# Kernel tuning notes

Hardware: AMD Instinct MI355X
Metric: run time of the kernel (lower is better)

Reference implementation:

```python
import jax, jax.numpy as jnp
from jax import lax
import numpy as np

SEQ, BATCH, IN, H = 512, 256, 180, 8


def _lstm_layer(x, w_ih, w_hh, b_ih, b_hh):
    # x: [S, B, I]; PyTorch gate order: i, f, g, o stacked along 4H
    S, B, _ = x.shape
    Hh = w_hh.shape[1]
    # input contribution for all timesteps at once (one big GEMM)
    xg = jnp.einsum('sbi,gi->sbg', x, w_ih) + b_ih + b_hh  # [S, B, 4H]

    def step(carry, xt):
        h, c = carry
        g = xt + h @ w_hh.T  # [B, 4H]
        i, f, gg, o = jnp.split(g, 4, axis=-1)
        i = jax.nn.sigmoid(i)
        f = jax.nn.sigmoid(f)
        gg = jnp.tanh(gg)
        o = jax.nn.sigmoid(o)
        c = f * c + i * gg
        h = o * jnp.tanh(c)
        return (h, c), h

    init = (jnp.zeros((B, Hh), x.dtype), jnp.zeros((B, Hh), x.dtype))
    _, ys = lax.scan(step, init, xg)
    return ys  # [S, B, H]


def setup_inputs() -> dict:
    key = jax.random.key(0)
    ks = jax.random.split(key, 11)
    s = 1.0 / np.sqrt(H)  # PyTorch LSTM init scale
    return {
        'x': jax.random.normal(ks[0], (SEQ, BATCH, IN), jnp.float32),
        'w_ih0': jax.random.uniform(ks[1], (4 * H, IN), jnp.float32, -s, s),
        'w_hh0': jax.random.uniform(ks[2], (4 * H, H), jnp.float32, -s, s),
        'b_ih0': jax.random.uniform(ks[3], (4 * H,), jnp.float32, -s, s),
        'b_hh0': jax.random.uniform(ks[4], (4 * H,), jnp.float32, -s, s),
        'w_ih1': jax.random.uniform(ks[5], (4 * H, H), jnp.float32, -s, s),
        'w_hh1': jax.random.uniform(ks[6], (4 * H, H), jnp.float32, -s, s),
        'b_ih1': jax.random.uniform(ks[7], (4 * H,), jnp.float32, -s, s),
        'b_hh1': jax.random.uniform(ks[8], (4 * H,), jnp.float32, -s, s),
        'w_reg': jax.random.uniform(ks[9], (2, H), jnp.float32, -s, s),
        'b_reg': jax.random.uniform(ks[10], (2,), jnp.float32, -s, s),
    }


def reference(x, w_ih0, w_hh0, b_ih0, b_hh0, w_ih1, w_hh1, b_ih1, b_hh1, w_reg, b_reg):
    h1 = _lstm_layer(x, w_ih0, w_hh0, b_ih0, b_hh0)   # [S, B, H]
    h2 = _lstm_layer(h1, w_ih1, w_hh1, b_ih1, b_hh1)  # [S, B, H]
    S, B, Hh = h2.shape
    flat = h2.reshape(S * B, Hh)
    return flat @ w_reg.T + b_reg  # [S*B, 2]
```

## Files before the change

### kernel.cpp

```cpp
#include <hip/hip_runtime.h>

#define S_  512
#define B_  256
#define NIN 180

typedef float v2 __attribute__((ext_vector_type(2)));

#define SSIG  -1.4426950408889634f
#define STANH -2.8853900817779268f

#define QP_X1 0xB1
#define QP_X2 0x4E
#define QP_X3 0x1B
#define ROR4  0x124
#define ROR8  0x128

template<int CTRL>
__device__ __forceinline__ float dppf(float x) {
    return __uint_as_float((unsigned)__builtin_amdgcn_update_dpp(
        0, (int)__float_as_uint(x), CTRL, 0xF, 0xF, true));
}

#define ROTS8(h, r) do { \
    r[0] = (h); \
    r[1] = dppf<QP_X1>(h); \
    r[2] = dppf<QP_X2>(h); \
    r[3] = dppf<QP_X3>(h); \
    r[4] = dppf<ROR4>(h); \
    r[5] = dppf<QP_X1>(r[4]); \
    r[6] = dppf<QP_X2>(r[4]); \
    r[7] = dppf<QP_X3>(r[4]); \
} while (0)

__global__ __launch_bounds__(512) void xg_gemm(
    const float* __restrict__ x, const float* __restrict__ w,
    const float* __restrict__ bi, const float* __restrict__ bh,
    float* __restrict__ xg2)
{
    __shared__ float xs[2][4][256];

    const int tid  = threadIdx.x;
    const int lane = tid & 63;
    const int qb   = __builtin_amdgcn_readfirstlane((tid >> 6) & 1);
    const int rs   = tid >> 7;
    const int row  = rs * 64 + lane;
    const int s    = blockIdx.x;
    const bool ldr = (tid < 256);

    const float* xrp = x + ((size_t)s * B_ + tid) * NIN;

    float acc[16];
    #pragma unroll
    for (int k = 0; k < 16; ++k) acc[k] = 0.f;

    float4 rr[4];
    float4 x0;
    if (ldr) {
        x0    = *(const float4*)(xrp + 0);
        rr[1] = *(const float4*)(xrp + 4);
        rr[2] = *(const float4*)(xrp + 8);
        rr[3] = *(const float4*)(xrp + 12);
        rr[0] = *(const float4*)(xrp + 16);
        xs[0][0][tid] = x0.x; xs[0][1][tid] = x0.y;
        xs[0][2][tid] = x0.z; xs[0][3][tid] = x0.w;
    }
    __syncthreads();

    auto COMP = [&](int ii, int buf) {
        float xe0 = xs[buf][0][row];
        float xe1 = xs[buf][1][row];
        float xe2 = xs[buf][2][row];
        float xe3 = xs[buf][3][row];
        #pragma unroll
        for (int jj = 0; jj < 8; ++jj) {
            float4 wA = *(const float4*)(w + (size_t)(qb * 8 + jj) * NIN + 4 * ii);
            float4 wB = *(const float4*)(w + (size_t)((2 + qb) * 8 + jj) * NIN + 4 * ii);
            acc[2*jj]   = __builtin_fmaf(wA.x, xe0, acc[2*jj]);
            acc[2*jj+1] = __builtin_fmaf(wB.x, xe0, acc[2*jj+1]);
            acc[2*jj]   = __builtin_fmaf(wA.y, xe1, acc[2*jj]);
            acc[2*jj+1] = __builtin_fmaf(wB.y, xe1, acc[2*jj+1]);
            acc[2*jj]   = __builtin_fmaf(wA.z, xe2, acc[2*jj]);
            acc[2*jj+1] = __builtin_fmaf(wB.z, xe2, acc[2*jj+1]);
            acc[2*jj]   = __builtin_fmaf(wA.w, xe3, acc[2*jj]);
            acc[2*jj+1] = __builtin_fmaf(wB.w, xe3, acc[2*jj+1]);
        }
    };

    for (int base = 0; base <= 40; base += 4) {
        #pragma unroll
        for (int p = 0; p < 4; ++p) {
            const int ii = base + p;
            if (ldr && ii < 44) {
                const int sl = (p + 1) & 3;
                float4 wv = rr[sl];
                xs[(ii + 1) & 1][0][tid] = wv.x;
                xs[(ii + 1) & 1][1][tid] = wv.y;
                xs[(ii + 1) & 1][2][tid] = wv.z;
                xs[(ii + 1) & 1][3][tid] = wv.w;
                if (ii <= 39)
                    rr[sl] = *(const float4*)(xrp + 4 * (ii + 5));
            }
            COMP(ii, p & 1);
            __syncthreads();
        }
    }
    COMP(44, 0);

    float ob[16];
    #pragma unroll
    for (int c = 0; c < 2; ++c) {
        #pragma unroll
        for (int jj = 0; jj < 8; ++jj) {
            int g = (qb + 2 * c) * 8 + jj;
            float sc = (qb == 0 && c == 1) ? STANH : SSIG;
            ob[2*jj+c] = sc * acc[2*jj+c] + sc * (bi[g] + bh[g]);
        }
    }
    float* dst = xg2 + (((size_t)s * 64 + (row >> 2)) * 64
                        + (row & 3) * 16 + qb * 8) * 2;
    #pragma unroll
    for (int k = 0; k < 4; ++k) {
        float4 o = {ob[4*k], ob[4*k+1], ob[4*k+2], ob[4*k+3]};
        *(float4*)(dst + 4 * k) = o;
    }
}

__global__ __launch_bounds__(256, 1) void lstm_scan(
    const float* __restrict__ xg,
    const float* __restrict__ w_hh0,
    const float* __restrict__ w_ih1, const float* __restrict__ w_hh1,
    const float* __restrict__ b_ih1, const float* __restrict__ b_hh1,
    const float* __restrict__ w_reg, const float* __restrict__ b_reg,
    float* __restrict__ out)
{
    __shared__ float ring0[16][64];
    __shared__ float ring1[16][128];
    __shared__ float ring2[16][64];

    const int tid = threadIdx.x;
    const int wid = tid >> 6;
    const int lt  = tid & 63;
    const int j   = lt & 7;
    const int b3  = (lt >> 3) & 1;
    const int cc  = lt >> 4;
    const bool b3z = (b3 == 0);
    const int bid = blockIdx.x;

    const int gA = b3 * 8 + j;
    const int gB = (2 + b3) * 8 + j;
    const float sB_ = b3z ? STANH : SSIG;
    const float aB  = b3z ? 2.0f : 1.0f;
    const float bB  = b3z ? -1.0f : 0.0f;

    auto COMBINE2 = [&](float tA, float tB, float& c, float& h) {
        float m  = tA * tB;
        float mr = dppf<ROR8>(m);
        float fa = dppf<ROR8>(tA);
        float ob = dppf<ROR8>(tB);
        float ig = b3z ? m  : mr;
        float f  = b3z ? fa : tA;
        float o  = b3z ? ob : tB;
        c = __builtin_fmaf(f, c, ig);
        float th = __builtin_fmaf(2.0f, __builtin_amdgcn_rcpf(
            1.0f + __builtin_amdgcn_exp2f(STANH * c)), -1.0f);
        h = o * th;
    };

    if (wid == 0) {
        v2 w0p[8];
        #pragma unroll
        for (int m = 0; m < 8; ++m) {
            int k = j ^ m;
            w0p[m] = v2{SSIG * w_hh0[gA * 8 + k], sB_ * w_hh0[gB * 8 + k]};
        }
        float h0p = 0.f, c0v = 0.f;

        const float* xbase = xg + (size_t)bid * 128 + lt * 2;
        v2 xq[8];
        #pragma unroll
        for (int k = 0; k < 8; ++k) xq[k] = *(const v2*)(xbase + (size_t)k * 8192);

        for (int hh = 0; hh < 64; ++hh) {
            const float* pre = xbase + (size_t)((8 * hh + 8) & 511) * 8192;
            const int sb8 = (hh & 1) * 8;
            #pragma unroll
            for (int k = 0; k < 8; ++k) {
                v2 xc = xq[k];
                xq[k] = *(const v2*)(pre + (size_t)k * 8192);
                float r0[8];
                ROTS8(h0p, r0);
                v2 a0L = __builtin_elementwise_fma(w0p[0], v2{r0[0], r0[0]}, xc);
                v2 a0H = w0p[4] * v2{r0[4], r0[4]};
                #pragma unroll
                for (int m = 1; m < 4; ++m) {
                    a0L = __builtin_elementwise_fma(w0p[m], v2{r0[m], r0[m]}, a0L);
                    a0H = __builtin_elementwise_fma(w0p[m + 4], v2{r0[m + 4], r0[m + 4]}, a0H);
                }
                v2 a0 = a0L + a0H;
                float eA = __builtin_amdgcn_exp2f(a0.x);
                float eB = __builtin_amdgcn_exp2f(a0.y);
                float tA = __builtin_amdgcn_rcpf(1.0f + eA);
                float tB = __builtin_fmaf(aB, __builtin_amdgcn_rcpf(1.0f + eB), bB);
                COMBINE2(tA, tB, c0v, h0p);
                ring0[sb8 + k][lt] = h0p;
                if (k == 3 || k == 7) __syncthreads();
            }
        }
        __syncthreads();
        __syncthreads();
    } else if (wid == 1) {
        v2 wi1p[8];
        #pragma unroll
        for (int m = 0; m < 8; ++m) {
            int k = j ^ m;
            wi1p[m] = v2{SSIG * w_ih1[gA * 8 + k], sB_ * w_ih1[gB * 8 + k]};
        }
        const v2 b1p = v2{SSIG * (b_ih1[gA] + b_hh1[gA]),
                          sB_  * (b_ih1[gB] + b_hh1[gB])};

        __syncthreads();
        for (int p = 1; p <= 128; ++p) {
            const int sb = ((p - 1) & 3) * 4;
            float h0v[4];
            #pragma unroll
            for (int k = 0; k < 4; ++k) h0v[k] = ring0[sb + k][lt];
            #pragma unroll
            for (int k = 0; k < 4; ++k) {
                float r0[8];
                ROTS8(h0v[k], r0);
                v2 a = __builtin_elementwise_fma(wi1p[0], v2{r0[0], r0[0]}, b1p);
                #pragma unroll
                for (int m = 1; m < 8; ++m)
                    a = __builtin_elementwise_fma(wi1p[m], v2{r0[m], r0[m]}, a);
                *(v2*)&ring1[sb + k][lt * 2] = a;
            }
            __syncthreads();
        }
        __syncthreads();
    } else if (wid == 2) {
        v2 wh1p[8];
        #pragma unroll
        for (int m = 0; m < 8; ++m) {
            int k = j ^ m;
            wh1p[m] = v2{SSIG * w_hh1[gA * 8 + k], sB_ * w_hh1[gB * 8 + k]};
        }
        float h1p = 0.f, c1v = 0.f;

        auto BODY4 = [&](int p) {
            const int sb = ((p - 2) & 3) * 4;
            v2 a1in[4];
            #pragma unroll
            for (int k = 0; k < 4; ++k) a1in[k] = *(const v2*)&ring1[sb + k][lt * 2];
            #pragma unroll
            for (int k = 0; k < 4; ++k) {
                float r1[8];
                ROTS8(h1p, r1);
                v2 aL = __builtin_elementwise_fma(wh1p[0], v2{r1[0], r1[0]}, a1in[k]);
                v2 aH = wh1p[4] * v2{r1[4], r1[4]};
                #pragma unroll
                for (int m = 1; m < 4; ++m) {
                    aL = __builtin_elementwise_fma(wh1p[m], v2{r1[m], r1[m]}, aL);
                    aH = __builtin_elementwise_fma(wh1p[m + 4], v2{r1[m + 4], r1[m + 4]}, aH);
                }
                v2 a1 = aL + aH;
                float eA = __builtin_amdgcn_exp2f(a1.x);
                float eB = __builtin_amdgcn_exp2f(a1.y);
                float tA = __builtin_amdgcn_rcpf(1.0f + eA);
                float tB = __builtin_fmaf(aB, __builtin_amdgcn_rcpf(1.0f + eB), bB);
                COMBINE2(tA, tB, c1v, h1p);
                ring2[sb + k][lt] = h1p;
            }
        };

        __syncthreads();
        __syncthreads();
        for (int p = 2; p <= 128; ++p) { BODY4(p); __syncthreads(); }
        BODY4(129);
        __syncthreads();
    } else {
        float wrl[8];
        #pragma unroll
        for (int m = 0; m < 8; ++m) wrl[m] = w_reg[b3 * 8 + (j ^ m)];
        const float br  = b_reg[b3];
        const bool isl  = (j == 0);
        const int  ooff = (bid * 4 + cc) * 2 + b3;

        auto PBODY = [&](int sb, int wbase) {
            float h1v[4];
            #pragma unroll
            for (int k = 0; k < 4; ++k) h1v[k] = ring2[sb + k][lt];
            #pragma unroll
            for (int k = 0; k < 4; ++k) {
                float r1[8];
                ROTS8(h1v[k], r1);
                float pp = br;
                #pragma unroll
                for (int m = 0; m < 8; ++m) pp = __builtin_fmaf(wrl[m], r1[m], pp);
                if (isl) out[(size_t)(wbase + k) * 512 + ooff] = pp;
            }
        };

        __syncthreads();
        __syncthreads();
        __syncthreads();
        for (int p = 3; p <= 129; ++p) {
            PBODY(((p - 3) & 3) * 4, 4 * (p - 3));
            __syncthreads();
        }
        PBODY(12, 508);
    }
}

extern "C" void kernel_launch(void* const* d_in, const int* in_sizes, int n_in,
                              void* d_out, int out_size, void* d_ws, size_t ws_size,
                              hipStream_t stream) {
    (void)in_sizes; (void)n_in; (void)out_size; (void)ws_size;
    const float* x     = (const float*)d_in[0];
    const float* w_ih0 = (const float*)d_in[1];
    const float* w_hh0 = (const float*)d_in[2];
    const float* b_ih0 = (const float*)d_in[3];
    const float* b_hh0 = (const float*)d_in[4];
    const float* w_ih1 = (const float*)d_in[5];
    const float* w_hh1 = (const float*)d_in[6];
    const float* b_ih1 = (const float*)d_in[7];
    const float* b_hh1 = (const float*)d_in[8];
    const float* w_reg = (const float*)d_in[9];
    const float* b_reg = (const float*)d_in[10];
    float* out = (float*)d_out;
    float* xg2 = (float*)d_ws;

    xg_gemm<<<512, 512, 0, stream>>>(x, w_ih0, b_ih0, b_hh0, xg2);
    lstm_scan<<<64, 256, 0, stream>>>(xg2, w_hh0, w_ih1, w_hh1, b_ih1, b_hh1,
                                      w_reg, b_reg, out);
}
```

Before: 136.5 us.

## Restructure input-projection GEMM: stage full 64-row x tile in LDS, 4x more blocks

The xg_gemm kernel now uses 2048 blocks, each covering 64 batch rows of one timestep. Each block loads the whole 64x180 x tile into padded shared memory once, instead of streaming 4-column slices double-buffered with a sync per slice. Each wave then computes 4 gate outputs per row with a single unsynchronized K loop. The aim is more parallelism and the removal of the per-slice barriers. In exchange, the x tile is read from LDS by all 8 waves (8x LDS reads), and the weights are loaded per wave from global memory or cache.

```diff
diff --git a/kernel.cpp b/kernel.cpp
--- a/kernel.cpp
+++ b/kernel.cpp
@@ -37,92 +37,76 @@
     const float* __restrict__ bi, const float* __restrict__ bh,
     float* __restrict__ xg2)
 {
-    __shared__ float xs[2][4][256];
-
-    const int tid  = threadIdx.x;
-    const int lane = tid & 63;
-    const int qb   = __builtin_amdgcn_readfirstlane((tid >> 6) & 1);
-    const int rs   = tid >> 7;
-    const int row  = rs * 64 + lane;
-    const int s    = blockIdx.x;
-    const bool ldr = (tid < 256);
-
-    const float* xrp = x + ((size_t)s * B_ + tid) * NIN;
-
-    float acc[16];
+    __shared__ float xs[64][181];
+
+    const int tid = threadIdx.x;
+    const int s   = blockIdx.x >> 2;
+    const int rq  = blockIdx.x & 3;
+    const int b0  = rq * 64;
+
+    const float* xsrc = x + ((size_t)s * B_ + b0) * NIN;
     #pragma unroll
-    for (int k = 0; k < 16; ++k) acc[k] = 0.f;
-
-    float4 rr[4];
-    float4 x0;
-    if (ldr) {
-        x0    = *(const float4*)(xrp + 0);
-        rr[1] = *(const float4*)(xrp + 4);
-        rr[2] = *(const float4*)(xrp + 8);
-        rr[3] = *(const float4*)(xrp + 12);
-        rr[0] = *(const float4*)(xrp + 16);
-        xs[0][0][tid] = x0.x; xs[0][1][tid] = x0.y;
-        xs[0][2][tid] = x0.z; xs[0][3][tid] = x0.w;
+    for (int k = 0; k < 6; ++k) {
+        int f4 = tid + k * 512;
+        if (f4 < 2880) {
+            float4 v = *(const float4*)(xsrc + 4 * (size_t)f4);
+            int row = f4 / 45;
+            int col = (f4 - row * 45) * 4;
+            xs[row][col]     = v.x;
+            xs[row][col + 1] = v.y;
+            xs[row][col + 2] = v.z;
+            xs[row][col + 3] = v.w;
+        }
     }
     __syncthreads();
 
-    auto COMP = [&](int ii, int buf) {
-        float xe0 = xs[buf][0][row];
-        float xe1 = xs[buf][1][row];
-        float xe2 = xs[buf][2][row];
-        float xe3 = xs[buf][3][row];
-        #pragma unroll
-        for (int jj = 0; jj < 8; ++jj) {
-            float4 wA = *(const float4*)(w + (size_t)(qb * 8 + jj) * NIN + 4 * ii);
-            float4 wB = *(const float4*)(w + (size_t)((2 + qb) * 8 + jj) * NIN + 4 * ii);
-            acc[2*jj]   = __builtin_fmaf(wA.x, xe0, acc[2*jj]);
-            acc[2*jj+1] = __builtin_fmaf(wB.x, xe0, acc[2*jj+1]);
-            acc[2*jj]   = __builtin_fmaf(wA.y, xe1, acc[2*jj]);
-            acc[2*jj+1] = __builtin_fmaf(wB.y, xe1, acc[2*jj+1]);
-            acc[2*jj]   = __builtin_fmaf(wA.z, xe2, acc[2*jj]);
-            acc[2*jj+1] = __builtin_fmaf(wB.z, xe2, acc[2*jj+1]);
-            acc[2*jj]   = __builtin_fmaf(wA.w, xe3, acc[2*jj]);
-            acc[2*jj+1] = __builtin_fmaf(wB.w, xe3, acc[2*jj+1]);
-        }
-    };
-
-    for (int base = 0; base <= 40; base += 4) {
-        #pragma unroll
-        for (int p = 0; p < 4; ++p) {
-            const int ii = base + p;
-            if (ldr && ii < 44) {
-                const int sl = (p + 1) & 3;
-                float4 wv = rr[sl];
-                xs[(ii + 1) & 1][0][tid] = wv.x;
-                xs[(ii + 1) & 1][1][tid] = wv.y;
-                xs[(ii + 1) & 1][2][tid] = wv.z;
-                xs[(ii + 1) & 1][3][tid] = wv.w;
-                if (ii <= 39)
-                    rr[sl] = *(const float4*)(xrp + 4 * (ii + 5));
-            }
-            COMP(ii, p & 1);
-            __syncthreads();
-        }
+    const int wv   = __builtin_amdgcn_readfirstlane(tid >> 6);
+    const int qb   = wv & 1;
+    const int j0   = (wv >> 1) * 2;
+    const int lane = tid & 63;
+    const int b    = b0 + lane;
+
+    const int gA0 = qb * 8 + j0;
+    const int gB0 = (2 + qb) * 8 + j0;
+    const float* wA0 = w + (size_t)gA0 * NIN;
+    const float* wA1 = wA0 + NIN;
+    const float* wB0 = w + (size_t)gB0 * NIN;
+    const float* wB1 = wB0 + NIN;
+
+    float a0 = 0.f, a1 = 0.f, a2 = 0.f, a3 = 0.f;
+    #pragma unroll 9
+    for (int ii = 0; ii < 45; ++ii) {
+        float x0 = xs[lane][4 * ii];
+        float x1 = xs[lane][4 * ii + 1];
+        float x2 = xs[lane][4 * ii + 2];
+        float x3 = xs[lane][4 * ii + 3];
+        float4 wa = *(const float4*)(wA0 + 4 * ii);
+        float4 wb = *(const float4*)(wB0 + 4 * ii);
+        float4 wc = *(const float4*)(wA1 + 4 * ii);
+        float4 wd = *(const float4*)(wB1 + 4 * ii);
+        a0 = __builtin_fmaf(wa.x, x0, a0); a0 = __builtin_fmaf(wa.y, x1, a0);
+        a0 = __builtin_fmaf(wa.z, x2, a0); a0 = __builtin_fmaf(wa.w, x3, a0);
+        a1 = __builtin_fmaf(wb.x, x0, a1); a1 = __builtin_fmaf(wb.y, x1, a1);
+        a1 = __builtin_fmaf(wb.z, x2, a1); a1 = __builtin_fmaf(wb.w, x3, a1);
+        a2 = __builtin_fmaf(wc.x, x0, a2); a2 = __builtin_fmaf(wc.y, x1, a2);
+        a2 = __builtin_fmaf(wc.z, x2, a2); a2 = __builtin_fmaf(wc.w, x3, a2);
+        a3 = __builtin_fmaf(wd.x, x0, a3); a3 = __builtin_fmaf(wd.y, x1, a3);
+        a3 = __builtin_fmaf(wd.z, x2, a3); a3 = __builtin_fmaf(wd.w, x3, a3);
     }
-    COMP(44, 0);
-
-    float ob[16];
-    #pragma unroll
-    for (int c = 0; c < 2; ++c) {
-        #pragma unroll
-        for (int jj = 0; jj < 8; ++jj) {
-            int g = (qb + 2 * c) * 8 + jj;
-            float sc = (qb == 0 && c == 1) ? STANH : SSIG;
-            ob[2*jj+c] = sc * acc[2*jj+c] + sc * (bi[g] + bh[g]);
-        }
-    }
-    float* dst = xg2 + (((size_t)s * 64 + (row >> 2)) * 64
-                        + (row & 3) * 16 + qb * 8) * 2;
-    #pragma unroll
-    for (int k = 0; k < 4; ++k) {
-        float4 o = {ob[4*k], ob[4*k+1], ob[4*k+2], ob[4*k+3]};
-        *(float4*)(dst + 4 * k) = o;
-    }
+
+    const float scB = (qb == 0) ? STANH : SSIG;
+    float bA0 = bi[gA0] + bh[gA0];
+    float bA1 = bi[gA0 + 1] + bh[gA0 + 1];
+    float bB0 = bi[gB0] + bh[gB0];
+    float bB1 = bi[gB0 + 1] + bh[gB0 + 1];
+    float4 o;
+    o.x = SSIG * (a0 + bA0);
+    o.y = scB  * (a1 + bB0);
+    o.z = SSIG * (a2 + bA1);
+    o.w = scB  * (a3 + bB1);
+    float* dst = xg2 + (((size_t)s * 64 + (b >> 2)) * 64
+                        + (b & 3) * 16 + qb * 8 + j0) * 2;
+    *(float4*)dst = o;
 }
 
 __global__ __launch_bounds__(256, 1) void lstm_scan(
@@ -329,7 +313,7 @@
     float* out = (float*)d_out;
     float* xg2 = (float*)d_ws;
 
-    xg_gemm<<<512, 512, 0, stream>>>(x, w_ih0, b_ih0, b_hh0, xg2);
+    xg_gemm<<<2048, 512, 0, stream>>>(x, w_ih0, b_ih0, b_hh0, xg2);
     lstm_scan<<<64, 256, 0, stream>>>(xg2, w_hh0, w_ih1, w_hh1, b_ih1, b_hh1,
                                       w_reg, b_reg, out);
 }
```

Result: faster. 114.3 us (-16.2%).
